# Kernel tuning notes

Hardware: AMD Instinct MI355X
Metric: run time of the kernel (lower is better)

Reference implementation:

```python
import jax, jax.numpy as jnp
import numpy as np

N_NODES = 50000
N_EDGES = 800000
D = 128
L = 3
BN_EPS = 1e-5


def _l2norm(x):
    # torch F.normalize(p=2, dim=-1): x / max(||x||, 1e-12)
    n = jnp.linalg.norm(x, axis=-1, keepdims=True)
    return x / jnp.maximum(n, 1e-12)


def setup_inputs() -> dict:
    key = jax.random.key(0)
    ks = jax.random.split(key, 5)
    x = jax.random.normal(ks[0], (N_NODES, D), dtype=jnp.float32)
    edge_index = jax.random.randint(ks[1], (2, N_EDGES), 0, N_NODES, dtype=jnp.int64)
    # stacked per-layer params; Linear stored as [in, out] (y = x @ W + b)
    W1 = jax.random.normal(ks[2], (L, D, D), dtype=jnp.float32) * 0.05
    W2 = jax.random.normal(ks[3], (L, D, D), dtype=jnp.float32) * 0.05
    b1 = jnp.zeros((L, D), jnp.float32)
    b2 = jnp.zeros((L, D), jnp.float32)
    gamma = jnp.ones((L, D), jnp.float32)
    beta = jnp.zeros((L, D), jnp.float32)
    eps = jnp.zeros((L,), jnp.float32)
    return {"x": x, "edge_index": edge_index, "W1": W1, "b1": b1,
            "gamma": gamma, "beta": beta, "W2": W2, "b2": b2, "eps": eps}


def _gin_layer(x, src, dst, W1, b1, g, be, W2, b2, eps):
    # message + scatter-add aggregation: sum_j x_j -> node i
    agg = jax.ops.segment_sum(x[src], dst, num_segments=N_NODES)
    # update(): L2 normalize aggregated messages
    agg = _l2norm(agg)
    # eps-weighted residual on L2-normalized root features
    out = agg + (1.0 + eps) * _l2norm(x)
    # MLP: Linear -> BatchNorm1d (training stats) -> ReLU -> Linear
    h = out @ W1 + b1
    mu = jnp.mean(h, axis=0)
    var = jnp.mean(jnp.square(h - mu), axis=0)  # biased var (torch BN training)
    h = g * (h - mu) * jax.lax.rsqrt(var + BN_EPS) + be
    h = jax.nn.relu(h)
    return h @ W2 + b2


def reference(x, edge_index, W1, b1, gamma, beta, W2, b2, eps):
    src, dst = edge_index[0], edge_index[1]
    for i in range(L):
        x = _gin_layer(x, src, dst, W1[i], b1[i], gamma[i], beta[i], W2[i], b2[i], eps[i])
        if i != L - 1:
            x = jax.nn.relu(x)
    return x
```

## Files before the change

kernel.cpp:

```cpp
#include <hip/hip_runtime.h>
#include <hip/hip_bf16.h>

#define N_NODES 50000
#define N_EDGES 800000
#define D 128
#define L_LAYERS 3
#define BN_EPS 1e-5f
#define NBUK 196
#define BIN_CHUNK 4096
#define NBIN_BLOCKS 196
#define BSTRIDE 5120
#define CSTRIDE 5376
#define AROW 68
#define NPART 8
#define PADOFF (N_NODES << 8)

typedef __attribute__((ext_vector_type(8))) short short8;
typedef __attribute__((ext_vector_type(4))) float floatx4;
typedef __attribute__((ext_vector_type(4))) unsigned uintx4;

__device__ __forceinline__ unsigned short f2bf(float f) {
    unsigned u = __builtin_bit_cast(unsigned, f);
    u += 0x7FFFu + ((u >> 16) & 1u);
    return (unsigned short)(u >> 16);
}
__device__ __forceinline__ float bf2f(unsigned short h) {
    unsigned u = ((unsigned)h) << 16;
    return __builtin_bit_cast(float, u);
}
__device__ __forceinline__ float bf2f_lo(unsigned p) {
    return __builtin_bit_cast(float, p << 16);
}
__device__ __forceinline__ float bf2f_hi(unsigned p) {
    return __builtin_bit_cast(float, p & 0xFFFF0000u);
}
__device__ __forceinline__ unsigned cvtpk(float lo, float hi) {
    unsigned r;
    asm("v_cvt_pk_bf16_f32 %0, %1, %2" : "=v"(r) : "v"(lo), "v"(hi));
    return r;
}

__device__ __forceinline__ int edge_at(const void* ei, const int* flag64, long long i) {
    if (*flag64) return (int)((const long long*)ei)[i];
    return ((const int*)ei)[i];
}

__global__ __launch_bounds__(256) void prep_kernel(const float* __restrict__ x,
        const void* __restrict__ ei, int* __restrict__ flag,
        const float* __restrict__ W1, const float* __restrict__ W2,
        short* __restrict__ Wp, unsigned short* __restrict__ xb,
        unsigned* __restrict__ zreg, int zwords) {
    int bid = blockIdx.x;
    int t = threadIdx.x;
    if (bid == 0) {
        __shared__ int nz;
        if (t == 0) nz = 0;
        __syncthreads();
        if (((const int*)ei)[2 * t + 1] != 0) atomicAdd(&nz, 1);
        __syncthreads();
        if (t == 0) *flag = (nz == 0) ? 1 : 0;
        for (int i = t; i < zwords; i += 256) zreg[i] = 0u;
        if (t < 64) ((unsigned*)(xb + (size_t)N_NODES * D))[t] = 0u;
    } else if (bid <= 48) {
        int tid = (bid - 1) * 256 + t;
        int mat = tid >> 11;
        int t2 = tid & 2047;
        int kt = t2 >> 9;
        int nt = (t2 >> 6) & 7;
        int lane = t2 & 63;
        const float* W = (mat < 3) ? (W1 + (size_t)mat * D * D)
                                   : (W2 + (size_t)(mat - 3) * D * D);
        int kbase = kt * 32 + (lane >> 4) * 8;
        int n = nt * 16 + (lane & 15);
        unsigned fw[4];
        #pragma unroll
        for (int j = 0; j < 4; j++)
            fw[j] = cvtpk(W[(kbase + 2 * j) * D + n], W[(kbase + 2 * j + 1) * D + n]);
        *(uint4*)(Wp + (size_t)mat * D * D + (size_t)t2 * 8) =
            make_uint4(fw[0], fw[1], fw[2], fw[3]);
    } else {
        long long i = (long long)((bid - 49) * 256 + t) * 4;
        float4 v = *(const float4*)(x + i);
        unsigned w0 = cvtpk(v.x, v.y);
        unsigned w1 = cvtpk(v.z, v.w);
        *(uint2*)(xb + i) = make_uint2(w0, w1);
    }
}

__global__ __launch_bounds__(256) void bin_kernel(const void* __restrict__ ei,
        const int* __restrict__ flag64, int* __restrict__ bucketCursor,
        unsigned* __restrict__ binned) {
    __shared__ int lhist[NBUK];
    __shared__ int gbase[NBUK];
    int t = threadIdx.x;
    for (int i = t; i < NBUK; i += 256) lhist[i] = 0;
    __syncthreads();

    int e0 = blockIdx.x * BIN_CHUNK;
    unsigned w[BIN_CHUNK / 256];
    short bkt[BIN_CHUNK / 256];
    short lidx[BIN_CHUNK / 256];
    #pragma unroll
    for (int i = 0; i < BIN_CHUNK / 256; i++) {
        int e = e0 + t + i * 256;
        if (e < N_EDGES) {
            int s = edge_at(ei, flag64, e);
            int d = edge_at(ei, flag64, (long long)N_EDGES + e);
            int b = d >> 8;
            w[i] = ((unsigned)s << 8) | (unsigned)(d & 255);
            bkt[i] = (short)b;
            lidx[i] = (short)atomicAdd(&lhist[b], 1);
        } else {
            bkt[i] = -1;
        }
    }
    __syncthreads();
    for (int i = t; i < NBUK; i += 256) {
        int c = lhist[i];
        gbase[i] = i * BSTRIDE + (c ? atomicAdd(&bucketCursor[i], c) : 0);
    }
    __syncthreads();
    #pragma unroll
    for (int i = 0; i < BIN_CHUNK / 256; i++) {
        if (bkt[i] >= 0)
            binned[gbase[bkt[i]] + (int)lidx[i]] = w[i];
    }
}

__global__ __launch_bounds__(256) void csr_build_kernel(const unsigned* __restrict__ binned,
        const int* __restrict__ bucketCursor, int* __restrict__ rowptr,
        int* __restrict__ bucketEnd, int* __restrict__ csr) {
    __shared__ int ls[256];
    __shared__ int lhist[256];
    __shared__ int lcur[256];
    int b = blockIdx.x, t = threadIdx.x;
    int n = bucketCursor[b];
    const unsigned* src = binned + (size_t)b * BSTRIDE;

    lhist[t] = 0;
    __syncthreads();
    for (int i = t; i < n; i += 256)
        atomicAdd(&lhist[src[i] & 255u], 1);
    __syncthreads();
    int c = lhist[t];
    int pc = (c + 3) & ~3;
    ls[t] = pc;
    __syncthreads();
    for (int off = 1; off < 256; off <<= 1) {
        int u = (t >= off) ? ls[t - off] : 0;
        __syncthreads();
        ls[t] += u;
        __syncthreads();
    }
    int excl = ls[t] - pc;
    int base = b * CSTRIDE;
    int dst = b * 256 + t;
    if (dst <= N_NODES) rowptr[dst] = base + excl;
    if (t == 0) bucketEnd[b] = base + ls[255];
    lcur[t] = excl;
    __syncthreads();
    for (int i = t; i < n; i += 256) {
        unsigned wv = src[i];
        int pos = atomicAdd(&lcur[wv & 255u], 1);
        csr[base + pos] = (int)(wv & 0xFFFFFF00u);
    }
    __syncthreads();
    for (int i = lcur[t]; i < excl + pc; i++)
        csr[base + i] = PADOFF;
}

__global__ __launch_bounds__(256, 8) void gather_gemm1_kernel(
        const unsigned short* __restrict__ xb,
        const int* __restrict__ rowptr, const int* __restrict__ csr,
        const int* __restrict__ bucketEnd,
        const float* __restrict__ epsArr, int layer,
        const short* __restrict__ Wp, const float* __restrict__ bB,
        unsigned* __restrict__ Hout,
        float* __restrict__ gsum, float* __restrict__ gsq) {
    __shared__ __attribute__((aligned(16))) unsigned lA[16 * AROW];
    __shared__ int wq;
    const char* xbase = (const char*)xb;
    int wave = threadIdx.x >> 6, lane = threadIdx.x & 63;
    unsigned po = (unsigned)(lane << 2);
    int r0 = blockIdx.x * 16;
    float eps1 = 1.0f + epsArr[layer];
    if (threadIdx.x == 0) wq = 0;
    __syncthreads();

#define EDGE4(J) { \
    unsigned o0 = (unsigned)__shfl((int)iv, (J) + 0) + po; \
    unsigned o1 = (unsigned)__shfl((int)iv, (J) + 1) + po; \
    unsigned o2 = (unsigned)__shfl((int)iv, (J) + 2) + po; \
    unsigned o3 = (unsigned)__shfl((int)iv, (J) + 3) + po; \
    unsigned p0 = *(const unsigned*)(xbase + o0); \
    unsigned p1 = *(const unsigned*)(xbase + o1); \
    unsigned p2 = *(const unsigned*)(xbase + o2); \
    unsigned p3 = *(const unsigned*)(xbase + o3); \
    a0 += bf2f_lo(p0); a1 += bf2f_hi(p0); \
    b0 += bf2f_lo(p1); b1 += bf2f_hi(p1); \
    c0 += bf2f_lo(p2); c1 += bf2f_hi(p2); \
    d0 += bf2f_lo(p3); d1 += bf2f_hi(p3); }

    for (;;) {
        int r;
        if (lane == 0) r = atomicAdd(&wq, 1);
        r = __shfl(r, 0);
        if (r >= 16) break;
        int row = r0 + r;
        int beg = rowptr[row];
        int end = ((row & 255) == 255) ? bucketEnd[row >> 8] : rowptr[row + 1];
        float a0 = 0.f, a1 = 0.f, b0 = 0.f, b1 = 0.f;
        float c0 = 0.f, c1 = 0.f, d0 = 0.f, d1 = 0.f;
        for (int base = beg; base < end; base += 64) {
            int n = end - base;
            if (n > 64) n = 64;
            unsigned iv = (lane < n) ? (unsigned)csr[base + lane] : (unsigned)PADOFF;
            int j = 0;
            for (; j + 16 <= n; j += 16) {
                EDGE4(j) EDGE4(j + 4) EDGE4(j + 8) EDGE4(j + 12)
            }
            for (; j < n; j += 4) {
                EDGE4(j)
            }
        }
        float ax = a0 + b0 + c0 + d0;
        float ay = a1 + b1 + c1 + d1;
        unsigned pself = *(const unsigned*)(xbase + (((unsigned)row << 8) + po));
        float xv0 = bf2f_lo(pself), xv1 = bf2f_hi(pself);
        float sa = ax * ax + ay * ay;
        float sx = xv0 * xv0 + xv1 * xv1;
        #pragma unroll
        for (int mm = 32; mm >= 1; mm >>= 1) {
            sa += __shfl_xor(sa, mm);
            sx += __shfl_xor(sx, mm);
        }
        float ra = 1.0f / fmaxf(sqrtf(sa), 1e-12f);
        float rx = eps1 / fmaxf(sqrtf(sx), 1e-12f);
        lA[r * AROW + lane] = cvtpk(ax * ra + xv0 * rx, ay * ra + xv1 * rx);
    }
#undef EDGE4
    __syncthreads();

    int m = lane & 15, g = lane >> 4;
    int nt0 = wave * 2, nt1 = nt0 + 1;
    short8 afr[4];
    #pragma unroll
    for (int kt = 0; kt < 4; kt++)
        afr[kt] = *(const short8*)(lA + m * AROW + kt * 16 + g * 4);
    __syncthreads();

    floatx4 acc0 = (floatx4){0.f, 0.f, 0.f, 0.f};
    floatx4 acc1 = (floatx4){0.f, 0.f, 0.f, 0.f};
    #pragma unroll
    for (int kt = 0; kt < 4; kt++) {
        short8 bf0 = *(const short8*)(Wp + (size_t)((kt * 8 + nt0) * 64 + lane) * 8);
        short8 bf1 = *(const short8*)(Wp + (size_t)((kt * 8 + nt1) * 64 + lane) * 8);
        acc0 = __builtin_amdgcn_mfma_f32_16x16x32_bf16(afr[kt], bf0, acc0, 0, 0, 0);
        acc1 = __builtin_amdgcn_mfma_f32_16x16x32_bf16(afr[kt], bf1, acc1, 0, 0, 0);
    }

    unsigned short* hlds = (unsigned short*)lA;
    float bc0 = bB[nt0 * 16 + m], bc1 = bB[nt1 * 16 + m];
    float s0 = 0.f, q0 = 0.f, s1 = 0.f, q1 = 0.f;
    #pragma unroll
    for (int r = 0; r < 4; r++) {
        int lrow = g * 4 + r;
        float h0 = acc0[r] + bc0;
        float h1 = acc1[r] + bc1;
        hlds[lrow * (AROW * 2) + nt0 * 16 + m] = f2bf(h0);
        hlds[lrow * (AROW * 2) + nt1 * 16 + m] = f2bf(h1);
        s0 += h0; q0 += h0 * h0;
        s1 += h1; q1 += h1 * h1;
    }
    s0 += __shfl_xor(s0, 16); s0 += __shfl_xor(s0, 32);
    q0 += __shfl_xor(q0, 16); q0 += __shfl_xor(q0, 32);
    s1 += __shfl_xor(s1, 16); s1 += __shfl_xor(s1, 32);
    q1 += __shfl_xor(q1, 16); q1 += __shfl_xor(q1, 32);
    if (lane < 16) {
        float* gs = gsum + (size_t)(blockIdx.x & (NPART - 1)) * D;
        float* gq = gsq + (size_t)(blockIdx.x & (NPART - 1)) * D;
        atomicAdd(&gs[nt0 * 16 + m], s0);
        atomicAdd(&gs[nt1 * 16 + m], s1);
        atomicAdd(&gq[nt0 * 16 + m], q0);
        atomicAdd(&gq[nt1 * 16 + m], q1);
    }
    __syncthreads();

    {
        int crow = threadIdx.x >> 4;
        int cq = threadIdx.x & 15;
        uint4 v = *(const uint4*)(lA + crow * AROW + cq * 4);
        *(uint4*)(Hout + (size_t)(r0 + crow) * 64 + cq * 4) = v;
    }
}

__global__ __launch_bounds__(256, 8) void gemm2_mid_kernel(const unsigned short* __restrict__ H,
        const float* __restrict__ gsum, const float* __restrict__ gsq,
        const float* __restrict__ gamma, const float* __restrict__ beta,
        const short* __restrict__ Wp, const float* __restrict__ b,
        unsigned* __restrict__ Yb16) {
    __shared__ float s_scale[D];
    __shared__ float s_shift[D];
    __shared__ unsigned so[64 * AROW];
    if (threadIdx.x < D) {
        int c = threadIdx.x;
        const float invN = 1.0f / (float)N_NODES;
        float su = 0.f, sq = 0.f;
        #pragma unroll
        for (int pp = 0; pp < NPART; pp++) {
            su += gsum[(size_t)pp * D + c];
            sq += gsq[(size_t)pp * D + c];
        }
        float mu = su * invN;
        float var = fmaxf(sq * invN - mu * mu, 0.f);
        float is = rsqrtf(var + BN_EPS);
        float sc = gamma[c] * is;
        s_scale[c] = sc;
        s_shift[c] = beta[c] - mu * sc;
    }
    __syncthreads();

    int wave = threadIdx.x >> 6, lane = threadIdx.x & 63;
    int r0 = blockIdx.x * 64;
    int m = lane & 15, g = lane >> 4;
    int arow = r0 + wave * 16 + m;
    bool valid = arow < N_NODES;

    short8 a[4];
    #pragma unroll
    for (int kt = 0; kt < 4; kt++) {
        int koff = kt * 32 + g * 8;
        if (valid) {
            short8 hv = *(const short8*)(H + (long long)arow * D + koff);
            unsigned aw[4];
            #pragma unroll
            for (int jj = 0; jj < 4; jj++) {
                float h0 = bf2f((unsigned short)hv[2 * jj]);
                float h1 = bf2f((unsigned short)hv[2 * jj + 1]);
                float v0 = fmaxf(h0 * s_scale[koff + 2 * jj] + s_shift[koff + 2 * jj], 0.f);
                float v1 = fmaxf(h1 * s_scale[koff + 2 * jj + 1] + s_shift[koff + 2 * jj + 1], 0.f);
                aw[jj] = cvtpk(v0, v1);
            }
            a[kt] = __builtin_bit_cast(short8, (uintx4){aw[0], aw[1], aw[2], aw[3]});
        } else {
            a[kt] = (short8)0;
        }
    }

    floatx4 acc[8];
    #pragma unroll
    for (int nt = 0; nt < 8; nt++) acc[nt] = (floatx4){0.f, 0.f, 0.f, 0.f};
    #pragma unroll
    for (int nt = 0; nt < 8; nt++) {
        #pragma unroll
        for (int kt = 0; kt < 4; kt++) {
            short8 bf = *(const short8*)(Wp + (size_t)((kt * 8 + nt) * 64 + lane) * 8);
            acc[nt] = __builtin_amdgcn_mfma_f32_16x16x32_bf16(a[kt], bf, acc[nt], 0, 0, 0);
        }
    }

    unsigned short* sos = (unsigned short*)so;
    #pragma unroll
    for (int nt = 0; nt < 8; nt++) {
        int col = nt * 16 + m;
        float bcol = b[col];
        #pragma unroll
        for (int r = 0; r < 4; r++) {
            int lrow = wave * 16 + g * 4 + r;
            sos[lrow * (AROW * 2) + col] = f2bf(fmaxf(acc[nt][r] + bcol, 0.f));
        }
    }
    __syncthreads();
    #pragma unroll
    for (int k = 0; k < 4; k++) {
        int c = threadIdx.x + k * 256;
        int crow = c >> 4;
        int cq = c & 15;
        if (r0 + crow < N_NODES) {
            uint4 v = *(const uint4*)(so + crow * AROW + cq * 4);
            *(uint4*)(Yb16 + (size_t)(r0 + crow) * 64 + cq * 4) = v;
        }
    }
}

__global__ __launch_bounds__(256, 4) void gemm2_final_kernel(const unsigned short* __restrict__ H,
        const float* __restrict__ gsum, const float* __restrict__ gsq,
        const float* __restrict__ gamma, const float* __restrict__ beta,
        const short* __restrict__ Wp, const float* __restrict__ b,
        float* __restrict__ Yf32) {
    __shared__ float s_scale[D];
    __shared__ float s_shift[D];
    __shared__ float sof[64 * 132];
    if (threadIdx.x < D) {
        int c = threadIdx.x;
        const float invN = 1.0f / (float)N_NODES;
        float su = 0.f, sq = 0.f;
        #pragma unroll
        for (int pp = 0; pp < NPART; pp++) {
            su += gsum[(size_t)pp * D + c];
            sq += gsq[(size_t)pp * D + c];
        }
        float mu = su * invN;
        float var = fmaxf(sq * invN - mu * mu, 0.f);
        float is = rsqrtf(var + BN_EPS);
        float sc = gamma[c] * is;
        s_scale[c] = sc;
        s_shift[c] = beta[c] - mu * sc;
    }
    __syncthreads();

    int wave = threadIdx.x >> 6, lane = threadIdx.x & 63;
    int r0 = blockIdx.x * 64;
    int m = lane & 15, g = lane >> 4;
    int arow = r0 + wave * 16 + m;
    bool valid = arow < N_NODES;

    short8 a[4];
    #pragma unroll
    for (int kt = 0; kt < 4; kt++) {
        int koff = kt * 32 + g * 8;
        if (valid) {
            short8 hv = *(const short8*)(H + (long long)arow * D + koff);
            unsigned aw[4];
            #pragma unroll
            for (int jj = 0; jj < 4; jj++) {
                float h0 = bf2f((unsigned short)hv[2 * jj]);
                float h1 = bf2f((unsigned short)hv[2 * jj + 1]);
                float v0 = fmaxf(h0 * s_scale[koff + 2 * jj] + s_shift[koff + 2 * jj], 0.f);
                float v1 = fmaxf(h1 * s_scale[koff + 2 * jj + 1] + s_shift[koff + 2 * jj + 1], 0.f);
                aw[jj] = cvtpk(v0, v1);
            }
            a[kt] = __builtin_bit_cast(short8, (uintx4){aw[0], aw[1], aw[2], aw[3]});
        } else {
            a[kt] = (short8)0;
        }
    }

    floatx4 acc[8];
    #pragma unroll
    for (int nt = 0; nt < 8; nt++) acc[nt] = (floatx4){0.f, 0.f, 0.f, 0.f};
    #pragma unroll
    for (int nt = 0; nt < 8; nt++) {
        #pragma unroll
        for (int kt = 0; kt < 4; kt++) {
            short8 bf = *(const short8*)(Wp + (size_t)((kt * 8 + nt) * 64 + lane) * 8);
            acc[nt] = __builtin_amdgcn_mfma_f32_16x16x32_bf16(a[kt], bf, acc[nt], 0, 0, 0);
        }
    }

    #pragma unroll
    for (int nt = 0; nt < 8; nt++) {
        int col = nt * 16 + m;
        float bcol = b[col];
        #pragma unroll
        for (int r = 0; r < 4; r++) {
            int lrow = wave * 16 + g * 4 + r;
            sof[lrow * 132 + col] = acc[nt][r] + bcol;
        }
    }
    __syncthreads();
    #pragma unroll
    for (int k = 0; k < 8; k++) {
        int c = threadIdx.x + k * 256;
        int crow = c >> 5;
        int cq = c & 31;
        if (r0 + crow < N_NODES) {
            float4 v = *(const float4*)(sof + crow * 132 + cq * 4);
            *(float4*)(Yf32 + (size_t)(r0 + crow) * D + cq * 4) = v;
        }
    }
}

extern "C" void kernel_launch(void* const* d_in, const int* in_sizes, int n_in,
                              void* d_out, int out_size, void* d_ws, size_t ws_size,
                              hipStream_t stream) {
    const float* x      = (const float*)d_in[0];
    const void*  ei     = d_in[1];
    const float* W1     = (const float*)d_in[2];
    const float* b1     = (const float*)d_in[3];
    const float* gamma  = (const float*)d_in[4];
    const float* beta   = (const float*)d_in[5];
    const float* W2     = (const float*)d_in[6];
    const float* b2     = (const float*)d_in[7];
    const float* epsArr = (const float*)d_in[8];
    float* out = (float*)d_out;

    char* ws = (char*)d_ws;
    const size_t xbuf = (size_t)(N_NODES + 1) * D * sizeof(short);
    const size_t hbuf = (size_t)N_NODES * D * sizeof(short);
    unsigned short* Xb  = (unsigned short*)ws;
    unsigned* H16       = (unsigned*)(ws + xbuf);
    char* p             = ws + xbuf + hbuf;
    short* Wp       = (short*)p;         p += 6 * (size_t)D * D * sizeof(short);
    int* rowptr     = (int*)p;           p += (N_NODES + 1) * sizeof(int);
    int* csr        = (int*)p;           p += (size_t)NBUK * CSTRIDE * sizeof(int);
    unsigned* binned= (unsigned*)p;      p += (size_t)NBUK * BSTRIDE * sizeof(unsigned);
    int* bucketEnd  = (int*)p;           p += NBUK * sizeof(int);
    int* flag       = (int*)p;           p += sizeof(int);
    char* zbase     = p;
    int* bucketCursor=(int*)p;           p += NBUK * sizeof(int);
    float* stats    = (float*)p;         p += (size_t)L_LAYERS * 2 * NPART * D * sizeof(float);
    int zwords      = (int)((p - zbase) / 4);

    prep_kernel<<<1 + 48 + (N_NODES * D / 4) / 256, 256, 0, stream>>>(
        x, ei, flag, W1, W2, Wp, Xb, (unsigned*)zbase, zwords);

    bin_kernel<<<NBIN_BLOCKS, 256, 0, stream>>>(ei, flag, bucketCursor, binned);
    csr_build_kernel<<<NBUK, 256, 0, stream>>>(binned, bucketCursor, rowptr, bucketEnd, csr);

    const int g1Grid = N_NODES / 16;
    const int g2Grid = (N_NODES + 63) / 64;
    for (int l = 0; l < L_LAYERS; l++) {
        float* gsum = stats + (size_t)l * 2 * NPART * D;
        float* gsq  = gsum + (size_t)NPART * D;

        gather_gemm1_kernel<<<g1Grid, 256, 0, stream>>>(
            Xb, rowptr, csr, bucketEnd, epsArr, l,
            Wp + (size_t)l * D * D, b1 + (size_t)l * D,
            H16, gsum, gsq);
        if (l == L_LAYERS - 1) {
            gemm2_final_kernel<<<g2Grid, 256, 0, stream>>>(
                (const unsigned short*)H16, gsum, gsq,
                gamma + (size_t)l * D, beta + (size_t)l * D,
                Wp + (size_t)(3 + l) * D * D, b2 + (size_t)l * D, out);
        } else {
            gemm2_mid_kernel<<<g2Grid, 256, 0, stream>>>(
                (const unsigned short*)H16, gsum, gsq,
                gamma + (size_t)l * D, beta + (size_t)l * D,
                Wp + (size_t)(3 + l) * D * D, b2 + (size_t)l * D, (unsigned*)Xb);
        }
    }
}
```

Before: 219.7 us.

## Split gather into feature-sliced planes and separate norm+GEMM1 kernel

Node features are now also stored as four 32-column bf16 planes, so each gather block handles one slice and keeps its working set small enough for cache reuse. The fused gather+GEMM1 kernel is split into a slice gather kernel that writes fp32 aggregates and a norm_gemm1 kernel that normalizes and runs the matmul. The split adds an fp32 agg round trip through memory, an extra launch per layer, and extra plane writes in prep and gemm2_mid. NPART is raised to spread the BN stat atomics.

```diff
diff --git a/kernel.cpp b/kernel.cpp
--- a/kernel.cpp
+++ b/kernel.cpp
@@ -12,8 +12,9 @@
 #define BSTRIDE 5120
 #define CSTRIDE 5376
 #define AROW 68
-#define NPART 8
-#define PADOFF (N_NODES << 8)
+#define NPART 16
+#define PLANE_BYTES ((size_t)(N_NODES + 1) * 64)
+#define PADOFFP (N_NODES << 6)
 
 typedef __attribute__((ext_vector_type(8))) short short8;
 typedef __attribute__((ext_vector_type(4))) float floatx4;
@@ -49,6 +50,7 @@
         const void* __restrict__ ei, int* __restrict__ flag,
         const float* __restrict__ W1, const float* __restrict__ W2,
         short* __restrict__ Wp, unsigned short* __restrict__ xb,
+        char* __restrict__ planes,
         unsigned* __restrict__ zreg, int zwords) {
     int bid = blockIdx.x;
     int t = threadIdx.x;
@@ -61,6 +63,10 @@
         if (t == 0) *flag = (nz == 0) ? 1 : 0;
         for (int i = t; i < zwords; i += 256) zreg[i] = 0u;
         if (t < 64) ((unsigned*)(xb + (size_t)N_NODES * D))[t] = 0u;
+        if (t >= 64 && t < 128) {
+            int s = (t - 64) >> 4, w = (t - 64) & 15;
+            ((unsigned*)(planes + (size_t)s * PLANE_BYTES))[(size_t)N_NODES * 16 + w] = 0u;
+        }
     } else if (bid <= 48) {
         int tid = (bid - 1) * 256 + t;
         int mat = tid >> 11;
@@ -84,6 +90,11 @@
         unsigned w0 = cvtpk(v.x, v.y);
         unsigned w1 = cvtpk(v.z, v.w);
         *(uint2*)(xb + i) = make_uint2(w0, w1);
+        int node = (int)(i >> 7);
+        int c0 = (int)(i & 127);
+        int s = c0 >> 5;
+        *(uint2*)(planes + (size_t)s * PLANE_BYTES + (size_t)node * 64 + (c0 & 31) * 2) =
+            make_uint2(w0, w1);
     }
 }
 
@@ -162,44 +173,27 @@
     for (int i = t; i < n; i += 256) {
         unsigned wv = src[i];
         int pos = atomicAdd(&lcur[wv & 255u], 1);
-        csr[base + pos] = (int)(wv & 0xFFFFFF00u);
+        csr[base + pos] = (int)((wv & 0xFFFFFF00u) >> 2);
     }
     __syncthreads();
     for (int i = lcur[t]; i < excl + pc; i++)
-        csr[base + i] = PADOFF;
-}
-
-__global__ __launch_bounds__(256, 8) void gather_gemm1_kernel(
-        const unsigned short* __restrict__ xb,
+        csr[base + i] = PADOFFP;
+}
+
+__global__ __launch_bounds__(256, 8) void slice_gather_kernel(
+        const char* __restrict__ planes,
         const int* __restrict__ rowptr, const int* __restrict__ csr,
         const int* __restrict__ bucketEnd,
-        const float* __restrict__ epsArr, int layer,
-        const short* __restrict__ Wp, const float* __restrict__ bB,
-        unsigned* __restrict__ Hout,
-        float* __restrict__ gsum, float* __restrict__ gsq) {
-    __shared__ __attribute__((aligned(16))) unsigned lA[16 * AROW];
+        float* __restrict__ agg) {
     __shared__ int wq;
-    const char* xbase = (const char*)xb;
-    int wave = threadIdx.x >> 6, lane = threadIdx.x & 63;
-    unsigned po = (unsigned)(lane << 2);
-    int r0 = blockIdx.x * 16;
-    float eps1 = 1.0f + epsArr[layer];
+    int slice = blockIdx.x & 3;
+    int r0 = (blockIdx.x >> 2) * 16;
+    const char* plane = planes + (size_t)slice * PLANE_BYTES;
+    int lane = threadIdx.x & 63;
+    int g = lane >> 4, p = lane & 15;
+    unsigned po = (unsigned)(p << 2);
     if (threadIdx.x == 0) wq = 0;
     __syncthreads();
-
-#define EDGE4(J) { \
-    unsigned o0 = (unsigned)__shfl((int)iv, (J) + 0) + po; \
-    unsigned o1 = (unsigned)__shfl((int)iv, (J) + 1) + po; \
-    unsigned o2 = (unsigned)__shfl((int)iv, (J) + 2) + po; \
-    unsigned o3 = (unsigned)__shfl((int)iv, (J) + 3) + po; \
-    unsigned p0 = *(const unsigned*)(xbase + o0); \
-    unsigned p1 = *(const unsigned*)(xbase + o1); \
-    unsigned p2 = *(const unsigned*)(xbase + o2); \
-    unsigned p3 = *(const unsigned*)(xbase + o3); \
-    a0 += bf2f_lo(p0); a1 += bf2f_hi(p0); \
-    b0 += bf2f_lo(p1); b1 += bf2f_hi(p1); \
-    c0 += bf2f_lo(p2); c1 += bf2f_hi(p2); \
-    d0 += bf2f_lo(p3); d1 += bf2f_hi(p3); }
 
     for (;;) {
         int r;
@@ -209,39 +203,94 @@
         int row = r0 + r;
         int beg = rowptr[row];
         int end = ((row & 255) == 255) ? bucketEnd[row >> 8] : rowptr[row + 1];
-        float a0 = 0.f, a1 = 0.f, b0 = 0.f, b1 = 0.f;
-        float c0 = 0.f, c1 = 0.f, d0 = 0.f, d1 = 0.f;
+        float a0 = 0.f, a1 = 0.f;
         for (int base = beg; base < end; base += 64) {
             int n = end - base;
             if (n > 64) n = 64;
-            unsigned iv = (lane < n) ? (unsigned)csr[base + lane] : (unsigned)PADOFF;
+            unsigned iv = (lane < n) ? (unsigned)csr[base + lane] : (unsigned)PADOFFP;
             int j = 0;
             for (; j + 16 <= n; j += 16) {
-                EDGE4(j) EDGE4(j + 4) EDGE4(j + 8) EDGE4(j + 12)
+                unsigned o0 = (unsigned)__shfl((int)iv, j + g) + po;
+                unsigned o1 = (unsigned)__shfl((int)iv, j + 4 + g) + po;
+                unsigned o2 = (unsigned)__shfl((int)iv, j + 8 + g) + po;
+                unsigned o3 = (unsigned)__shfl((int)iv, j + 12 + g) + po;
+                unsigned p0 = *(const unsigned*)(plane + o0);
+                unsigned p1 = *(const unsigned*)(plane + o1);
+                unsigned p2 = *(const unsigned*)(plane + o2);
+                unsigned p3 = *(const unsigned*)(plane + o3);
+                a0 += bf2f_lo(p0); a1 += bf2f_hi(p0);
+                a0 += bf2f_lo(p1); a1 += bf2f_hi(p1);
+                a0 += bf2f_lo(p2); a1 += bf2f_hi(p2);
+                a0 += bf2f_lo(p3); a1 += bf2f_hi(p3);
             }
             for (; j < n; j += 4) {
-                EDGE4(j)
+                unsigned o0 = (unsigned)__shfl((int)iv, j + g) + po;
+                unsigned p0 = *(const unsigned*)(plane + o0);
+                a0 += bf2f_lo(p0); a1 += bf2f_hi(p0);
             }
         }
-        float ax = a0 + b0 + c0 + d0;
-        float ay = a1 + b1 + c1 + d1;
-        unsigned pself = *(const unsigned*)(xbase + (((unsigned)row << 8) + po));
-        float xv0 = bf2f_lo(pself), xv1 = bf2f_hi(pself);
-        float sa = ax * ax + ay * ay;
-        float sx = xv0 * xv0 + xv1 * xv1;
-        #pragma unroll
-        for (int mm = 32; mm >= 1; mm >>= 1) {
+        a0 += __shfl_xor(a0, 16); a0 += __shfl_xor(a0, 32);
+        a1 += __shfl_xor(a1, 16); a1 += __shfl_xor(a1, 32);
+        if (g == 0) {
+            unsigned long long pv =
+                ((unsigned long long)__builtin_bit_cast(unsigned, a1) << 32) |
+                (unsigned long long)__builtin_bit_cast(unsigned, a0);
+            *(unsigned long long*)(agg + (size_t)row * D + slice * 32 + p * 2) = pv;
+        }
+    }
+}
+
+__global__ __launch_bounds__(256, 8) void norm_gemm1_kernel(
+        const unsigned short* __restrict__ xb,
+        const float* __restrict__ agg,
+        const float* __restrict__ epsArr, int layer,
+        const short* __restrict__ Wp, const float* __restrict__ bB,
+        unsigned* __restrict__ Hout,
+        float* __restrict__ gsum, float* __restrict__ gsq) {
+    __shared__ __attribute__((aligned(16))) unsigned lA[16 * AROW];
+    const char* xbase = (const char*)xb;
+    int wave = threadIdx.x >> 6, lane = threadIdx.x & 63;
+    int g = lane >> 4, p = lane & 15;
+    int r0 = blockIdx.x * 16;
+    float eps1 = 1.0f + epsArr[layer];
+    int rw2 = threadIdx.x >> 4, pq2 = threadIdx.x & 15;
+
+    uint4 sv = *(const uint4*)(xbase + (((unsigned)(r0 + rw2)) << 8) + (pq2 << 4));
+    const float* ap = agg + (size_t)(r0 + rw2) * D + pq2 * 8;
+    float4 q0 = *(const float4*)ap;
+    float4 q1 = *(const float4*)(ap + 4);
+
+    {
+        float s[8];
+        s[0] = q0.x; s[1] = q0.y; s[2] = q0.z; s[3] = q0.w;
+        s[4] = q1.x; s[5] = q1.y; s[6] = q1.z; s[7] = q1.w;
+        float xv[8];
+        xv[0] = bf2f_lo(sv.x); xv[1] = bf2f_hi(sv.x);
+        xv[2] = bf2f_lo(sv.y); xv[3] = bf2f_hi(sv.y);
+        xv[4] = bf2f_lo(sv.z); xv[5] = bf2f_hi(sv.z);
+        xv[6] = bf2f_lo(sv.w); xv[7] = bf2f_hi(sv.w);
+        float sa = 0.f, sx = 0.f;
+        #pragma unroll
+        for (int k = 0; k < 8; k++) { sa += s[k] * s[k]; sx += xv[k] * xv[k]; }
+        #pragma unroll
+        for (int mm = 8; mm >= 1; mm >>= 1) {
             sa += __shfl_xor(sa, mm);
             sx += __shfl_xor(sx, mm);
         }
         float ra = 1.0f / fmaxf(sqrtf(sa), 1e-12f);
         float rx = eps1 / fmaxf(sqrtf(sx), 1e-12f);
-        lA[r * AROW + lane] = cvtpk(ax * ra + xv0 * rx, ay * ra + xv1 * rx);
-    }
-#undef EDGE4
-    __syncthreads();
-
-    int m = lane & 15, g = lane >> 4;
+        float o[8];
+        #pragma unroll
+        for (int k = 0; k < 8; k++) o[k] = s[k] * ra + xv[k] * rx;
+        unsigned w0 = cvtpk(o[0], o[1]);
+        unsigned w1 = cvtpk(o[2], o[3]);
+        unsigned w2 = cvtpk(o[4], o[5]);
+        unsigned w3 = cvtpk(o[6], o[7]);
+        *(uint4*)(lA + rw2 * AROW + pq2 * 4) = make_uint4(w0, w1, w2, w3);
+    }
+    __syncthreads();
+
+    int m = p;
     int nt0 = wave * 2, nt1 = nt0 + 1;
     short8 afr[4];
     #pragma unroll
@@ -261,7 +310,7 @@
 
     unsigned short* hlds = (unsigned short*)lA;
     float bc0 = bB[nt0 * 16 + m], bc1 = bB[nt1 * 16 + m];
-    float s0 = 0.f, q0 = 0.f, s1 = 0.f, q1 = 0.f;
+    float s0 = 0.f, q0s = 0.f, s1 = 0.f, q1s = 0.f;
     #pragma unroll
     for (int r = 0; r < 4; r++) {
         int lrow = g * 4 + r;
@@ -269,20 +318,20 @@
         float h1 = acc1[r] + bc1;
         hlds[lrow * (AROW * 2) + nt0 * 16 + m] = f2bf(h0);
         hlds[lrow * (AROW * 2) + nt1 * 16 + m] = f2bf(h1);
-        s0 += h0; q0 += h0 * h0;
-        s1 += h1; q1 += h1 * h1;
+        s0 += h0; q0s += h0 * h0;
+        s1 += h1; q1s += h1 * h1;
     }
     s0 += __shfl_xor(s0, 16); s0 += __shfl_xor(s0, 32);
-    q0 += __shfl_xor(q0, 16); q0 += __shfl_xor(q0, 32);
+    q0s += __shfl_xor(q0s, 16); q0s += __shfl_xor(q0s, 32);
     s1 += __shfl_xor(s1, 16); s1 += __shfl_xor(s1, 32);
-    q1 += __shfl_xor(q1, 16); q1 += __shfl_xor(q1, 32);
+    q1s += __shfl_xor(q1s, 16); q1s += __shfl_xor(q1s, 32);
     if (lane < 16) {
         float* gs = gsum + (size_t)(blockIdx.x & (NPART - 1)) * D;
         float* gq = gsq + (size_t)(blockIdx.x & (NPART - 1)) * D;
         atomicAdd(&gs[nt0 * 16 + m], s0);
         atomicAdd(&gs[nt1 * 16 + m], s1);
-        atomicAdd(&gq[nt0 * 16 + m], q0);
-        atomicAdd(&gq[nt1 * 16 + m], q1);
+        atomicAdd(&gq[nt0 * 16 + m], q0s);
+        atomicAdd(&gq[nt1 * 16 + m], q1s);
     }
     __syncthreads();
 
@@ -298,7 +347,7 @@
         const float* __restrict__ gsum, const float* __restrict__ gsq,
         const float* __restrict__ gamma, const float* __restrict__ beta,
         const short* __restrict__ Wp, const float* __restrict__ b,
-        unsigned* __restrict__ Yb16) {
+        unsigned* __restrict__ Yb16, char* __restrict__ planes) {
     __shared__ float s_scale[D];
     __shared__ float s_shift[D];
     __shared__ unsigned so[64 * AROW];
@@ -381,6 +430,18 @@
             *(uint4*)(Yb16 + (size_t)(r0 + crow) * 64 + cq * 4) = v;
         }
     }
+    {
+        int prow = threadIdx.x >> 2;
+        int q = threadIdx.x & 3;
+        if (r0 + prow < N_NODES) {
+            #pragma unroll
+            for (int s = 0; s < 4; s++) {
+                uint4 v = *(const uint4*)(so + prow * AROW + s * 16 + q * 4);
+                *(uint4*)(planes + (size_t)s * PLANE_BYTES +
+                          (size_t)(r0 + prow) * 64 + q * 16) = v;
+            }
+        }
+    }
 }
 
 __global__ __launch_bounds__(256, 4) void gemm2_final_kernel(const unsigned short* __restrict__ H,
@@ -491,7 +552,9 @@
     unsigned short* Xb  = (unsigned short*)ws;
     unsigned* H16       = (unsigned*)(ws + xbuf);
     char* p             = ws + xbuf + hbuf;
+    char* planes    = p;                 p += 4 * PLANE_BYTES;
     short* Wp       = (short*)p;         p += 6 * (size_t)D * D * sizeof(short);
+    float* agg      = (float*)p;         p += (size_t)N_NODES * D * sizeof(float);
     int* rowptr     = (int*)p;           p += (N_NODES + 1) * sizeof(int);
     int* csr        = (int*)p;           p += (size_t)NBUK * CSTRIDE * sizeof(int);
     unsigned* binned= (unsigned*)p;      p += (size_t)NBUK * BSTRIDE * sizeof(unsigned);
@@ -503,19 +566,22 @@
     int zwords      = (int)((p - zbase) / 4);
 
     prep_kernel<<<1 + 48 + (N_NODES * D / 4) / 256, 256, 0, stream>>>(
-        x, ei, flag, W1, W2, Wp, Xb, (unsigned*)zbase, zwords);
+        x, ei, flag, W1, W2, Wp, Xb, planes, (unsigned*)zbase, zwords);
 
     bin_kernel<<<NBIN_BLOCKS, 256, 0, stream>>>(ei, flag, bucketCursor, binned);
     csr_build_kernel<<<NBUK, 256, 0, stream>>>(binned, bucketCursor, rowptr, bucketEnd, csr);
 
+    const int sgGrid = (N_NODES / 16) * 4;
     const int g1Grid = N_NODES / 16;
     const int g2Grid = (N_NODES + 63) / 64;
     for (int l = 0; l < L_LAYERS; l++) {
         float* gsum = stats + (size_t)l * 2 * NPART * D;
         float* gsq  = gsum + (size_t)NPART * D;
 
-        gather_gemm1_kernel<<<g1Grid, 256, 0, stream>>>(
-            Xb, rowptr, csr, bucketEnd, epsArr, l,
+        slice_gather_kernel<<<sgGrid, 256, 0, stream>>>(
+            planes, rowptr, csr, bucketEnd, agg);
+        norm_gemm1_kernel<<<g1Grid, 256, 0, stream>>>(
+            Xb, agg, epsArr, l,
             Wp + (size_t)l * D * D, b1 + (size_t)l * D,
             H16, gsum, gsq);
         if (l == L_LAYERS - 1) {
@@ -527,7 +593,8 @@
             gemm2_mid_kernel<<<g2Grid, 256, 0, stream>>>(
                 (const unsigned short*)H16, gsum, gsq,
                 gamma + (size_t)l * D, beta + (size_t)l * D,
-                Wp + (size_t)(3 + l) * D * D, b2 + (size_t)l * D, (unsigned*)Xb);
-        }
-    }
-}
+                Wp + (size_t)(3 + l) * D * D, b2 + (size_t)l * D,
+                (unsigned*)Xb, planes);
+        }
+    }
+}
```

Result: slower. 279.0 us (+27.0%).
